# Optimization experiments

Hardware: AMD Instinct MI355X
Metric: run time of the kernel (lower is better)

## Reference

```python
import jax, jax.numpy as jnp
import numpy as np

B, S, D, H, DFF = 4, 2048, 1024, 16, 4096
DK = D // H
EPS = 1e-9


def setup_inputs() -> dict:
    key = jax.random.key(0)
    ks = jax.random.split(key, 12)
    s = lambda k, shape, scale: jax.random.normal(k, shape, dtype=jnp.float32) * scale
    return {
        "x": s(ks[0], (B, S, D), 1.0),
        "mask": jnp.ones((B, 1, 1, S), dtype=jnp.int32),
        # Linear weights stored torch-style [out, in]
        "wq": s(ks[1], (D, D), D ** -0.5),
        "wk": s(ks[2], (D, D), D ** -0.5),
        "wv": s(ks[3], (D, D), D ** -0.5),
        "wo": s(ks[4], (D, D), D ** -0.5),
        "w1": s(ks[5], (DFF, D), D ** -0.5),
        "b1": jnp.zeros((DFF,), jnp.float32),
        "w2": s(ks[6], (D, DFF), DFF ** -0.5),
        "b2": jnp.zeros((D,), jnp.float32),
        "g1": jnp.ones((D,), jnp.float32),
        "be1": jnp.zeros((D,), jnp.float32),
        "g2": jnp.ones((D,), jnp.float32),
        "be2": jnp.zeros((D,), jnp.float32),
    }


def _layernorm(x, gamma, beta):
    # Matches AddAndNorm: torch.std uses Bessel correction (ddof=1)
    mean = jnp.mean(x, axis=-1, keepdims=True)
    var = jnp.sum((x - mean) ** 2, axis=-1, keepdims=True) / (x.shape[-1] - 1)
    return gamma * (x - mean) / jnp.sqrt(var + EPS) + beta


def _mha(x, mask, wq, wk, wv, wo):
    b, s, d = x.shape
    def proj(w):  # [b,s,d] @ [d,d]^T -> heads [b,h,s,dk]
        return (x @ w.T).reshape(b, s, H, DK).transpose(0, 2, 1, 3)
    q, k, v = proj(wq), proj(wk), proj(wv)
    scores = jnp.einsum("bhqd,bhkd->bhqk", q, k) / jnp.sqrt(jnp.float32(DK))
    scores = jnp.where(mask == 0, jnp.float32(-1e9), scores)
    attn = jax.nn.softmax(scores, axis=-1)
    out = jnp.einsum("bhqk,bhkd->bhqd", attn, v)
    out = out.transpose(0, 2, 1, 3).reshape(b, s, d)
    return out @ wo.T


def reference(x, mask, wq, wk, wv, wo, w1, b1, w2, b2, g1, be1, g2, be2):
    # Residual 1: x + MHA(LN(x))  (dropout = 0)
    h1 = x + _mha(_layernorm(x, g1, be1), mask, wq, wk, wv, wo)
    # Residual 2: h1 + FFN(LN(h1))
    z = _layernorm(h1, g2, be2)
    ffn = jax.nn.relu(z @ w1.T + b1) @ w2.T + b2
    return h1 + ffn
```

## Files before the change

kernel.cpp:

```cpp
#include <hip/hip_runtime.h>
#include <hip/hip_bf16.h>
#include <cstdint>
#include <cstddef>

typedef __attribute__((ext_vector_type(8))) short short8;
typedef __attribute__((ext_vector_type(4))) float floatx4;
typedef __attribute__((ext_vector_type(4))) unsigned short ushort4e;

#define B_   4
#define S_   2048
#define D_   1024
#define H_   16
#define DK_  64
#define DFF_ 4096
#define MTOT (B_ * S_)
#define QKVLD 3072

__device__ __forceinline__ float bf2f(unsigned short u) {
    union { unsigned int i; float f; } v; v.i = ((unsigned int)u) << 16; return v.f;
}
__device__ __forceinline__ unsigned short f2bf(float f) {
    union { float f; unsigned int i; } v; v.f = f;
    unsigned int u = v.i;
    u += 0x7fffu + ((u >> 16) & 1u);
    return (unsigned short)(u >> 16);
}
__device__ __forceinline__ unsigned int pkbf(float a, float b) {
    union { float f; unsigned int u; } x, y; x.f = a; y.f = b;
    return ((x.u + 0x8000u) >> 16) | ((y.u + 0x8000u) & 0xffff0000u);
}
__device__ __forceinline__ void async_cp16(const void* g, void* l) {
    __builtin_amdgcn_global_load_lds(
        (const __attribute__((address_space(1))) unsigned int*)g,
        (__attribute__((address_space(3))) unsigned int*)l,
        16, 0, 0);
}

__global__ void dtype_probe(const unsigned short* __restrict__ x, int* flag) {
    __shared__ float red[4];
    const int tid = threadIdx.x;
    float mx = 0.f;
    #pragma unroll
    for (int i = 0; i < 16; i++) {
        float v = fabsf(bf2f(x[tid * 16 + i]));
        if (v != v) v = 1e30f;
        mx = fmaxf(mx, v);
    }
    #pragma unroll
    for (int off = 32; off > 0; off >>= 1) mx = fmaxf(mx, __shfl_down(mx, off));
    if ((tid & 63) == 0) red[tid >> 6] = mx;
    __syncthreads();
    if (tid == 0) {
        float m = fmaxf(fmaxf(red[0], red[1]), fmaxf(red[2], red[3]));
        *flag = (m > 50.f) ? 1 : 0;
    }
}

__device__ __forceinline__ void cvt8(const void* src, unsigned short* dst, int i, int fl) {
    if (fl) {
        const floatx4* s = (const floatx4*)src;
        floatx4 a = s[i * 2], b = s[i * 2 + 1];
        short8 o;
        o[0] = (short)f2bf(a[0]); o[1] = (short)f2bf(a[1]);
        o[2] = (short)f2bf(a[2]); o[3] = (short)f2bf(a[3]);
        o[4] = (short)f2bf(b[0]); o[5] = (short)f2bf(b[1]);
        o[6] = (short)f2bf(b[2]); o[7] = (short)f2bf(b[3]);
        ((short8*)dst)[i] = o;
    } else {
        ((short8*)dst)[i] = ((const short8*)src)[i];
    }
}

__global__ void cvt_kernel(const void* __restrict__ src,
                           unsigned short* __restrict__ dst,
                           int n8, const int* __restrict__ flag) {
    const int i = blockIdx.x * 256 + threadIdx.x;
    if (i >= n8) return;
    cvt8(src, dst, i, *flag);
}

__global__ void cvt4_kernel(const void* s0, const void* s1, const void* s2, const void* s3,
                            unsigned short* __restrict__ dst,
                            const int* __restrict__ flag) {
    const int t = blockIdx.x >> 9;
    const int i = (blockIdx.x & 511) * 256 + threadIdx.x;
    const void* s = (t == 0) ? s0 : (t == 1) ? s1 : (t == 2) ? s2 : s3;
    cvt8(s, dst + (size_t)t * (D_ * D_), i, *flag);
}

__global__ void cvt_small(const void* b1, const void* b2, const void* g1,
                          const void* be1, const void* g2, const void* be2,
                          unsigned short* db1, unsigned short* db2, unsigned short* dg1,
                          unsigned short* dbe1, unsigned short* dg2, unsigned short* dbe2,
                          const int* __restrict__ flag) {
    const int fl = *flag;
    for (int i = threadIdx.x; i < 1152; i += 256) {
        if (i < 512)       cvt8(b1,  db1,  i,        fl);
        else if (i < 640)  cvt8(b2,  db2,  i - 512,  fl);
        else if (i < 768)  cvt8(g1,  dg1,  i - 640,  fl);
        else if (i < 896)  cvt8(be1, dbe1, i - 768,  fl);
        else if (i < 1024) cvt8(g2,  dg2,  i - 896,  fl);
        else               cvt8(be2, dbe2, i - 1024, fl);
    }
}

#define BM 128
#define BN 128
#define BK 64

template<int RELU, int HAS_BIAS, int RES_MODE, int OUT_MODE>
__global__ __launch_bounds__(256)
void gemm_bt(const unsigned short* __restrict__ A, int lda,
             const unsigned short* __restrict__ W, int ldw,
             const unsigned short* __restrict__ bias,
             const void* resid,
             void* out,
             int M, int N, int K,
             const int* __restrict__ flagp)
{
    __shared__ unsigned short As[BM * BK];
    __shared__ unsigned short Bs[BN * BK];

    const int tid  = threadIdx.x;
    const int lane = tid & 63;
    const int wave = tid >> 6;
    const int wm = wave >> 1;
    const int wn = wave & 1;
    const int lr = lane & 15;
    const int lq = lane >> 4;

    const int m0 = blockIdx.y * BM;
    const int n0 = blockIdx.x * BN;

    int fl = 1;
    if (RES_MODE == 3 || OUT_MODE == 2) fl = *flagp;

    floatx4 acc[4][4];
    #pragma unroll
    for (int i = 0; i < 4; i++)
        #pragma unroll
        for (int j = 0; j < 4; j++)
            acc[i][j] = (floatx4){0.f, 0.f, 0.f, 0.f};

    const int lrow = lane >> 3;
    const int swz  = ((lane & 7) ^ lrow) * 8;
    const int rx   = lr & 7;
    const int p0   = ((lq)     ^ rx) * 8;
    const int p1   = ((4 + lq) ^ rx) * 8;

    for (int k0 = 0; k0 < K; k0 += BK) {
        #pragma unroll
        for (int t = 0; t < 4; t++) {
            const int row = wave * 32 + t * 8;
            async_cp16(A + (size_t)(m0 + row + lrow) * lda + k0 + swz, &As[row * BK]);
            async_cp16(W + (size_t)(n0 + row + lrow) * ldw + k0 + swz, &Bs[row * BK]);
        }
        __syncthreads();
        #pragma unroll
        for (int kk = 0; kk < 2; kk++) {
            const int pos = kk ? p1 : p0;
            short8 af[4], bfr[4];
            #pragma unroll
            for (int i = 0; i < 4; i++) {
                af[i]  = *(const short8*)(&As[(wm * 64 + i * 16 + lr) * BK + pos]);
                bfr[i] = *(const short8*)(&Bs[(wn * 64 + i * 16 + lr) * BK + pos]);
            }
            #pragma unroll
            for (int i = 0; i < 4; i++)
                #pragma unroll
                for (int j = 0; j < 4; j++)
                    acc[i][j] = __builtin_amdgcn_mfma_f32_16x16x32_bf16(
                                    af[i], bfr[j], acc[i][j], 0, 0, 0);
        }
        __syncthreads();
    }

    #pragma unroll
    for (int i = 0; i < 4; i++) {
        #pragma unroll
        for (int j = 0; j < 4; j++) {
            const int col = n0 + wn * 64 + j * 16 + lr;
            const float bv = HAS_BIAS ? bf2f(bias[col]) : 0.f;
            #pragma unroll
            for (int r = 0; r < 4; r++) {
                const int row = m0 + wm * 64 + i * 16 + lq * 4 + r;
                const size_t idx = (size_t)row * N + col;
                float vvv = acc[i][j][r] + bv;
                if (RES_MODE == 1) vvv += bf2f(((const unsigned short*)resid)[idx]);
                if (RES_MODE == 2) vvv += ((const float*)resid)[idx];
                if (RES_MODE == 3) vvv += fl ? ((const float*)resid)[idx]
                                             : bf2f(((const unsigned short*)resid)[idx]);
                if (RELU) vvv = fmaxf(vvv, 0.f);
                if (OUT_MODE == 1)      ((float*)out)[idx] = vvv;
                else if (OUT_MODE == 0) ((unsigned short*)out)[idx] = f2bf(vvv);
                else { if (fl) ((float*)out)[idx] = vvv;
                       else    ((unsigned short*)out)[idx] = f2bf(vvv); }
            }
        }
    }
}

template<int IN_MODE>
__global__ __launch_bounds__(256)
void ln_kernel(const void* __restrict__ Xv,
               const unsigned short* __restrict__ g,
               const unsigned short* __restrict__ be,
               unsigned short* __restrict__ out,
               const int* __restrict__ flagp)
{
    const int row = blockIdx.x;
    const int tid = threadIdx.x;
    int fl = 1;
    if (IN_MODE == 2) fl = *flagp;
    float x4[4];
    if (IN_MODE == 1 || fl) {
        const float* X = (const float*)Xv + (size_t)row * D_ + tid * 4;
        floatx4 t = *(const floatx4*)X;
        x4[0] = t[0]; x4[1] = t[1]; x4[2] = t[2]; x4[3] = t[3];
    } else {
        const unsigned short* X = (const unsigned short*)Xv + (size_t)row * D_ + tid * 4;
        ushort4e u = *(const ushort4e*)X;
        #pragma unroll
        for (int i = 0; i < 4; i++) x4[i] = bf2f(u[i]);
    }
    float s1 = x4[0] + x4[1] + x4[2] + x4[3];
    float s2 = x4[0]*x4[0] + x4[1]*x4[1] + x4[2]*x4[2] + x4[3]*x4[3];
    #pragma unroll
    for (int off = 32; off > 0; off >>= 1) {
        s1 += __shfl_down(s1, off);
        s2 += __shfl_down(s2, off);
    }
    __shared__ float r1[4], r2[4];
    const int wv = tid >> 6;
    if ((tid & 63) == 0) { r1[wv] = s1; r2[wv] = s2; }
    __syncthreads();
    s1 = r1[0] + r1[1] + r1[2] + r1[3];
    s2 = r2[0] + r2[1] + r2[2] + r2[3];
    const float mean = s1 * (1.0f / D_);
    const float var  = (s2 - (float)D_ * mean * mean) * (1.0f / (D_ - 1));
    const float rstd = rsqrtf(var + 1e-9f);

    ushort4e o4;
    #pragma unroll
    for (int i = 0; i < 4; i++) {
        const float gv = bf2f(g[tid * 4 + i]);
        const float bv = bf2f(be[tid * 4 + i]);
        o4[i] = f2bf(gv * (x4[i] - mean) * rstd + bv);
    }
    *(ushort4e*)(out + (size_t)row * D_ + tid * 4) = o4;
}

__global__ __launch_bounds__(256)
void vtrans(const unsigned short* __restrict__ V, int ldv,
            unsigned short* __restrict__ Vt)
{
    __shared__ unsigned short t[64 * 72];
    const int tid = threadIdx.x;
    const int kt  = blockIdx.x * 64;
    const int bh  = blockIdx.y;
    const int b   = bh >> 4, h = bh & 15;
    const int r   = tid >> 2;
    const int c4  = (tid & 3) * 16;
    const unsigned short* vp = V + (size_t)(b * S_ + kt + r) * ldv + h * DK_ + c4;
    *(short8*)&t[r * 72 + c4]     = *(const short8*)vp;
    *(short8*)&t[r * 72 + c4 + 8] = *(const short8*)(vp + 8);
    __syncthreads();
    short8 o0, o1;
    #pragma unroll
    for (int e = 0; e < 8; e++) {
        o0[e] = (short)t[(c4 + e) * 72 + r];
        o1[e] = (short)t[(c4 + 8 + e) * 72 + r];
    }
    unsigned short* op = Vt + ((size_t)bh * DK_ + r) * S_ + kt + c4;
    *(short8*)op       = o0;
    *(short8*)(op + 8) = o1;
}

#define ATK   64
#define KS_LD 64
#define PS_LD 72

__global__ __launch_bounds__(256)
void attn_mfma(const unsigned short* __restrict__ QKV,
               const unsigned short* __restrict__ Vt,
               const int* __restrict__ mask,
               unsigned short* __restrict__ ctx)
{
    __shared__ unsigned short Ks[ATK * KS_LD];
    __shared__ unsigned short Vts[DK_ * KS_LD];
    __shared__ unsigned short Ps[4][32 * PS_LD];
    __shared__ float maskadd[ATK];
    __shared__ float ared[4][32];

    const int tid  = threadIdx.x;
    const int lane = tid & 63;
    const int w    = tid >> 6;
    const int c    = lane & 15;
    const int qd   = lane >> 4;
    const int bh   = blockIdx.y;
    const int b    = bh >> 4;
    const int h    = bh & 15;
    const int q0   = blockIdx.x * 128 + w * 32;

    const int lrow = lane >> 3;
    const int swz  = ((lane & 7) ^ lrow) * 8;
    const int cx   = c & 7;

    const float QS = 0.18033688f;
    short8 qf[2][2];
    #pragma unroll
    for (int jq = 0; jq < 2; jq++)
        #pragma unroll
        for (int kk = 0; kk < 2; kk++) {
            const unsigned short* qp =
                QKV + (size_t)(b * S_ + q0 + jq * 16 + c) * QKVLD + h * DK_ + kk * 32 + qd * 8;
            short8 t = *(const short8*)qp;
            short8 o;
            #pragma unroll
            for (int e = 0; e < 8; e++)
                o[e] = (short)f2bf(bf2f((unsigned short)t[e]) * QS);
            qf[jq][kk] = o;
        }

    floatx4 acc_o[2][4];
    #pragma unroll
    for (int iq = 0; iq < 2; iq++)
        #pragma unroll
        for (int jd = 0; jd < 4; jd++)
            acc_o[iq][jd] = (floatx4){0.f, 0.f, 0.f, 0.f};
    float lrun[2] = {0.f, 0.f};

    for (int kt = 0; kt < S_; kt += ATK) {
        {
            const unsigned short* kbase =
                QKV + 1024 + (size_t)(b * S_ + kt + w * 16) * QKVLD + h * DK_;
            const unsigned short* vbase =
                Vt + ((size_t)bh * DK_ + w * 16) * S_ + kt;
            #pragma unroll
            for (int t = 0; t < 2; t++) {
                async_cp16(kbase + (size_t)(t * 8 + lrow) * QKVLD + swz,
                           &Ks[(w * 16 + t * 8) * KS_LD]);
                async_cp16(vbase + (size_t)(t * 8 + lrow) * S_ + swz,
                           &Vts[(w * 16 + t * 8) * KS_LD]);
            }
            if (tid < ATK) maskadd[tid] = (mask[b * S_ + kt + tid] == 0) ? -1e9f : 0.f;
        }
        __syncthreads();

        floatx4 acc_s[4][2];
        #pragma unroll
        for (int i = 0; i < 4; i++)
            #pragma unroll
            for (int jq = 0; jq < 2; jq++)
                acc_s[i][jq] = (floatx4){0.f, 0.f, 0.f, 0.f};
        #pragma unroll
        for (int kk = 0; kk < 2; kk++) {
            const int pos = ((kk * 4 + qd) ^ cx) * 8;
            short8 kf[4];
            #pragma unroll
            for (int i = 0; i < 4; i++)
                kf[i] = *(const short8*)&Ks[(i * 16 + c) * KS_LD + pos];
            #pragma unroll
            for (int i = 0; i < 4; i++)
                #pragma unroll
                for (int jq = 0; jq < 2; jq++)
                    acc_s[i][jq] = __builtin_amdgcn_mfma_f32_16x16x32_bf16(
                                       kf[i], qf[jq][kk], acc_s[i][jq], 0, 0, 0);
        }

        floatx4 madd[4];
        #pragma unroll
        for (int i = 0; i < 4; i++)
            madd[i] = *(const floatx4*)&maskadd[i * 16 + qd * 4];

        #pragma unroll
        for (int jq = 0; jq < 2; jq++) {
            float ps = 0.f;
            #pragma unroll
            for (int i = 0; i < 4; i++) {
                #pragma unroll
                for (int r = 0; r < 4; r++) {
                    float p = __builtin_amdgcn_exp2f(acc_s[i][jq][r] + madd[i][r]);
                    acc_s[i][jq][r] = p;
                    ps += p;
                }
                uint2 pk;
                pk.x = pkbf(acc_s[i][jq][0], acc_s[i][jq][1]);
                pk.y = pkbf(acc_s[i][jq][2], acc_s[i][jq][3]);
                *(uint2*)&Ps[w][(jq * 16 + c) * PS_LD + i * 16 + qd * 4] = pk;
            }
            ps += __shfl_xor(ps, 16);
            ps += __shfl_xor(ps, 32);
            lrun[jq] += ps;
        }

        #pragma unroll
        for (int kk = 0; kk < 2; kk++) {
            const int pos = ((kk * 4 + qd) ^ cx) * 8;
            short8 pf[2], vf[4];
            #pragma unroll
            for (int iq = 0; iq < 2; iq++)
                pf[iq] = *(const short8*)&Ps[w][(iq * 16 + c) * PS_LD + kk * 32 + qd * 8];
            #pragma unroll
            for (int jd = 0; jd < 4; jd++)
                vf[jd] = *(const short8*)&Vts[(jd * 16 + c) * KS_LD + pos];
            #pragma unroll
            for (int iq = 0; iq < 2; iq++)
                #pragma unroll
                for (int jd = 0; jd < 4; jd++)
                    acc_o[iq][jd] = __builtin_amdgcn_mfma_f32_16x16x32_bf16(
                                        pf[iq], vf[jd], acc_o[iq][jd], 0, 0, 0);
        }
        __syncthreads();
    }

    if (lane < 16) { ared[w][c] = 1.f / lrun[0]; ared[w][16 + c] = 1.f / lrun[1]; }
    floatx4 lv0 = *(const floatx4*)&ared[w][qd * 4];
    floatx4 lv1 = *(const floatx4*)&ared[w][16 + qd * 4];
    #pragma unroll
    for (int iq = 0; iq < 2; iq++)
        #pragma unroll
        for (int jd = 0; jd < 4; jd++)
            #pragma unroll
            for (int r = 0; r < 4; r++) {
                const int row = q0 + iq * 16 + qd * 4 + r;
                const int col = h * DK_ + jd * 16 + c;
                const float inv = (iq == 0) ? lv0[r] : lv1[r];
                ctx[(size_t)(b * S_ + row) * D_ + col] = f2bf(acc_o[iq][jd][r] * inv);
            }
}

extern "C" void kernel_launch(void* const* d_in, const int* in_sizes, int n_in,
                              void* d_out, int out_size, void* d_ws, size_t ws_size,
                              hipStream_t stream)
{
    const void* x_raw  = d_in[0];
    const int*  mask   = (const int*)d_in[1];
    const void* wq_raw = d_in[2];
    const void* wk_raw = d_in[3];
    const void* wv_raw = d_in[4];
    const void* wo_raw = d_in[5];
    const void* w1_raw = d_in[6];
    const void* b1_raw = d_in[7];
    const void* w2_raw = d_in[8];
    const void* b2_raw = d_in[9];
    const void* g1_raw = d_in[10];
    const void* be1_raw= d_in[11];
    const void* g2_raw = d_in[12];
    const void* be2_raw= d_in[13];

    char* ws = (char*)d_ws;
    const size_t MB = 1024 * 1024;
    int* flag = (int*)ws;
    unsigned short* cb1  = (unsigned short*)(ws + 1 * 1024);
    unsigned short* cb2  = (unsigned short*)(ws + 16 * 1024);
    unsigned short* cg1  = (unsigned short*)(ws + 32 * 1024);
    unsigned short* cbe1 = (unsigned short*)(ws + 40 * 1024);
    unsigned short* cg2  = (unsigned short*)(ws + 48 * 1024);
    unsigned short* cbe2 = (unsigned short*)(ws + 56 * 1024);
    unsigned short* cwqkvo = (unsigned short*)(ws + 1 * MB);
    unsigned short* cwqkv  = cwqkvo;
    unsigned short* cwo    = cwqkvo + 3 * (D_ * D_);
    unsigned short* cw1  = (unsigned short*)(ws + 9 * MB);
    unsigned short* cw2  = (unsigned short*)(ws + 17 * MB);
    unsigned short* xn1  = (unsigned short*)(ws + 25 * MB);
    unsigned short* ctx  = (unsigned short*)(ws + 25 * MB);
    unsigned short* zbuf = (unsigned short*)(ws + 25 * MB);
    unsigned short* qkv  = (unsigned short*)(ws + 41 * MB);
    float*          h1   = (float*)(ws + 57 * MB);
    unsigned short* vt   = (unsigned short*)d_out;
    unsigned short* xn2  = (unsigned short*)d_out;

    dtype_probe<<<1, 256, 0, stream>>>((const unsigned short*)x_raw, flag);
    cvt_small<<<1, 256, 0, stream>>>(b1_raw, b2_raw, g1_raw, be1_raw, g2_raw, be2_raw,
                                     cb1, cb2, cg1, cbe1, cg2, cbe2, flag);
    cvt4_kernel<<<2048, 256, 0, stream>>>(wq_raw, wk_raw, wv_raw, wo_raw, cwqkvo, flag);
    cvt_kernel<<<(DFF_ * D_ / 8 + 255) / 256, 256, 0, stream>>>(w1_raw, cw1, DFF_ * D_ / 8, flag);
    cvt_kernel<<<(D_ * DFF_ / 8 + 255) / 256, 256, 0, stream>>>(w2_raw, cw2, D_ * DFF_ / 8, flag);

    const dim3 blk(256);
    const dim3 gs(D_ / BN, MTOT / BM);
    const dim3 gsq(QKVLD / BN, MTOT / BM);
    const dim3 gs2(2048 / BN, MTOT / BM);

    ln_kernel<2><<<MTOT, blk, 0, stream>>>(x_raw, cg1, cbe1, xn1, flag);
    gemm_bt<0,0,0,0><<<gsq, blk, 0, stream>>>(xn1, D_, cwqkv, D_, nullptr, nullptr, qkv, MTOT, QKVLD, D_, flag);
    vtrans<<<dim3(S_ / 64, B_ * H_), blk, 0, stream>>>(qkv + 2048, QKVLD, vt);
    attn_mfma<<<dim3(S_ / 128, B_ * H_), blk, 0, stream>>>(qkv, vt, mask, ctx);
    gemm_bt<0,0,3,1><<<gs, blk, 0, stream>>>(ctx, D_, cwo, D_, nullptr, x_raw, h1, MTOT, D_, D_, flag);
    ln_kernel<1><<<MTOT, blk, 0, stream>>>(h1, cg2, cbe2, xn2, flag);
    gemm_bt<1,1,0,0><<<gs2, blk, 0, stream>>>(xn2, D_, cw1, D_, cb1, nullptr, zbuf, MTOT, 2048, D_, flag);
    gemm_bt<0,0,2,1><<<gs, blk, 0, stream>>>(zbuf, 2048, cw2, DFF_, nullptr, h1, h1, MTOT, D_, 2048, flag);
    const unsigned short* w1c = cw1 + (size_t)2048 * D_;
    gemm_bt<1,1,0,0><<<gs2, blk, 0, stream>>>(xn2, D_, w1c, D_, cb1 + 2048, nullptr, zbuf, MTOT, 2048, D_, flag);
    gemm_bt<0,1,2,2><<<gs, blk, 0, stream>>>(zbuf, 2048, cw2 + 2048, DFF_, cb2, h1, d_out, MTOT, D_, 2048, flag);
}
```

Measured before the change: 591.3 us.

## Double-buffer K/V tiles in attention and preload mask, remap blocks

Adds a second LDS buffer for K and V so the next tile's async copies are issued before computing the current tile, with explicit vmcnt waits and raw barriers replacing the per-iteration syncthreads. The whole mask row is converted to additive form once at kernel start instead of per tile. Block indices are remapped so consecutive blocks are spread across heads, which may help cache or XCD locality. MFMA sections get raised wave priority. LDS use grows (8KB mask plus a second K/V buffer), which may reduce occupancy. The hardcoded vmcnt count depends on how async_cp16 is issued.

```diff
diff --git a/kernel.cpp b/kernel.cpp
--- a/kernel.cpp
+++ b/kernel.cpp
@@ -6,6 +6,7 @@
 typedef __attribute__((ext_vector_type(8))) short short8;
 typedef __attribute__((ext_vector_type(4))) float floatx4;
 typedef __attribute__((ext_vector_type(4))) unsigned short ushort4e;
+typedef __attribute__((ext_vector_type(4))) int intx4;
 
 #define B_   4
 #define S_   2048
@@ -279,6 +280,7 @@
 #define ATK   64
 #define KS_LD 64
 #define PS_LD 72
+#define NT_   (S_ / ATK)
 
 __global__ __launch_bounds__(256)
 void attn_mfma(const unsigned short* __restrict__ QKV,
@@ -286,10 +288,10 @@
                const int* __restrict__ mask,
                unsigned short* __restrict__ ctx)
 {
-    __shared__ unsigned short Ks[ATK * KS_LD];
-    __shared__ unsigned short Vts[DK_ * KS_LD];
+    __shared__ unsigned short Ks[2][ATK * KS_LD];
+    __shared__ unsigned short Vts[2][DK_ * KS_LD];
     __shared__ unsigned short Ps[4][32 * PS_LD];
-    __shared__ float maskadd[ATK];
+    __shared__ float maskadd[S_];
     __shared__ float ared[4][32];
 
     const int tid  = threadIdx.x;
@@ -297,14 +299,32 @@
     const int w    = tid >> 6;
     const int c    = lane & 15;
     const int qd   = lane >> 4;
-    const int bh   = blockIdx.y;
+
+    const int flat    = blockIdx.y * gridDim.x + blockIdx.x;
+    const int logical = (flat & 7) * 128 + (flat >> 3);
+    const int bh   = logical >> 4;
     const int b    = bh >> 4;
     const int h    = bh & 15;
-    const int q0   = blockIdx.x * 128 + w * 32;
+    const int q0   = (logical & 15) * 128 + w * 32;
 
     const int lrow = lane >> 3;
     const int swz  = ((lane & 7) ^ lrow) * 8;
     const int cx   = c & 7;
+
+    {
+        const intx4* mp = (const intx4*)(mask + (size_t)b * S_);
+        intx4 m0 = mp[tid * 2];
+        intx4 m1 = mp[tid * 2 + 1];
+        float* dst = &maskadd[tid * 8];
+        dst[0] = (m0[0] == 0) ? -1e9f : 0.f;
+        dst[1] = (m0[1] == 0) ? -1e9f : 0.f;
+        dst[2] = (m0[2] == 0) ? -1e9f : 0.f;
+        dst[3] = (m0[3] == 0) ? -1e9f : 0.f;
+        dst[4] = (m1[0] == 0) ? -1e9f : 0.f;
+        dst[5] = (m1[1] == 0) ? -1e9f : 0.f;
+        dst[6] = (m1[2] == 0) ? -1e9f : 0.f;
+        dst[7] = (m1[3] == 0) ? -1e9f : 0.f;
+    }
 
     const float QS = 0.18033688f;
     short8 qf[2][2];
@@ -330,22 +350,33 @@
             acc_o[iq][jd] = (floatx4){0.f, 0.f, 0.f, 0.f};
     float lrun[2] = {0.f, 0.f};
 
-    for (int kt = 0; kt < S_; kt += ATK) {
-        {
-            const unsigned short* kbase =
-                QKV + 1024 + (size_t)(b * S_ + kt + w * 16) * QKVLD + h * DK_;
-            const unsigned short* vbase =
-                Vt + ((size_t)bh * DK_ + w * 16) * S_ + kt;
-            #pragma unroll
-            for (int t = 0; t < 2; t++) {
-                async_cp16(kbase + (size_t)(t * 8 + lrow) * QKVLD + swz,
-                           &Ks[(w * 16 + t * 8) * KS_LD]);
-                async_cp16(vbase + (size_t)(t * 8 + lrow) * S_ + swz,
-                           &Vts[(w * 16 + t * 8) * KS_LD]);
-            }
-            if (tid < ATK) maskadd[tid] = (mask[b * S_ + kt + tid] == 0) ? -1e9f : 0.f;
-        }
-        __syncthreads();
+    auto STAGE = [&](int buf, int kt) {
+        const unsigned short* kbase =
+            QKV + 1024 + (size_t)(b * S_ + kt + w * 16) * QKVLD + h * DK_;
+        const unsigned short* vbase =
+            Vt + ((size_t)bh * DK_ + w * 16) * S_ + kt;
+        #pragma unroll
+        for (int t = 0; t < 2; t++) {
+            async_cp16(kbase + (size_t)(t * 8 + lrow) * QKVLD + swz,
+                       &Ks[buf][(w * 16 + t * 8) * KS_LD]);
+            async_cp16(vbase + (size_t)(t * 8 + lrow) * S_ + swz,
+                       &Vts[buf][(w * 16 + t * 8) * KS_LD]);
+        }
+    };
+
+    __syncthreads();
+    STAGE(0, 0);
+
+    for (int t = 0; t < NT_; t++) {
+        const int cur = t & 1;
+        const int kt  = t * ATK;
+        if (t + 1 < NT_) {
+            STAGE(cur ^ 1, kt + ATK);
+            asm volatile("s_waitcnt vmcnt(4)" ::: "memory");
+        } else {
+            asm volatile("s_waitcnt vmcnt(0)" ::: "memory");
+        }
+        __builtin_amdgcn_s_barrier();
 
         floatx4 acc_s[4][2];
         #pragma unroll
@@ -359,19 +390,21 @@
             short8 kf[4];
             #pragma unroll
             for (int i = 0; i < 4; i++)
-                kf[i] = *(const short8*)&Ks[(i * 16 + c) * KS_LD + pos];
+                kf[i] = *(const short8*)&Ks[cur][(i * 16 + c) * KS_LD + pos];
+            __builtin_amdgcn_s_setprio(1);
             #pragma unroll
             for (int i = 0; i < 4; i++)
                 #pragma unroll
                 for (int jq = 0; jq < 2; jq++)
                     acc_s[i][jq] = __builtin_amdgcn_mfma_f32_16x16x32_bf16(
                                        kf[i], qf[jq][kk], acc_s[i][jq], 0, 0, 0);
+            __builtin_amdgcn_s_setprio(0);
         }
 
         floatx4 madd[4];
         #pragma unroll
         for (int i = 0; i < 4; i++)
-            madd[i] = *(const floatx4*)&maskadd[i * 16 + qd * 4];
+            madd[i] = *(const floatx4*)&maskadd[kt + i * 16 + qd * 4];
 
         #pragma unroll
         for (int jq = 0; jq < 2; jq++) {
@@ -403,15 +436,19 @@
                 pf[iq] = *(const short8*)&Ps[w][(iq * 16 + c) * PS_LD + kk * 32 + qd * 8];
             #pragma unroll
             for (int jd = 0; jd < 4; jd++)
-                vf[jd] = *(const short8*)&Vts[(jd * 16 + c) * KS_LD + pos];
+                vf[jd] = *(const short8*)&Vts[cur][(jd * 16 + c) * KS_LD + pos];
+            __builtin_amdgcn_s_setprio(1);
             #pragma unroll
             for (int iq = 0; iq < 2; iq++)
                 #pragma unroll
                 for (int jd = 0; jd < 4; jd++)
                     acc_o[iq][jd] = __builtin_amdgcn_mfma_f32_16x16x32_bf16(
                                         pf[iq], vf[jd], acc_o[iq][jd], 0, 0, 0);
-        }
-        __syncthreads();
+            __builtin_amdgcn_s_setprio(0);
+        }
+
+        asm volatile("" ::: "memory");
+        __builtin_amdgcn_s_barrier();
     }
 
     if (lane < 16) { ared[w][c] = 1.f / lrun[0]; ared[w][16 + c] = 1.f / lrun[1]; }
```

New measurement: 604.0 us. 1.02x slower.
